# Optimization experiments

Measured on AMD Instinct MI355X. Metric: run time of the kernel, lower is better.

The kernel has to match this reference:

```python
import jax, jax.numpy as jnp
import numpy as np

KERNEL = 11  # matches AttnBlock(kernel_size=11)
EPS = 1e-4


def _patches(x, k):
    """Extract k x k patches (stride 1, VALID), matching nn.Unfold ordering.

    x: [B, C, H, W] -> ([B, L, C*k*k], (Hp, Wp)) with L = Hp*Wp.
    """
    p = jax.lax.conv_general_dilated_patches(x, (k, k), (1, 1), 'VALID')  # [B, C*k*k, Hp, Wp]
    B, D, Hp, Wp = p.shape
    return p.reshape(B, D, Hp * Wp).transpose(0, 2, 1), (Hp, Wp)


def setup_inputs() -> dict:
    key = jax.random.key(0)
    k1, k2 = jax.random.split(key)
    im1 = jax.random.normal(k1, (4, 64, 40, 40), dtype=jnp.float32)
    im2 = jax.random.normal(k2, (4, 64, 40, 40), dtype=jnp.float32)
    return {"im1": im1, "im2": im2}


def reference(im1, im2):
    k = KERNEL
    # Dynamic per-sample filters from im1 patches, L2-normalized per patch.
    p1, _ = _patches(im1, k)                                  # [B, L, D], D = C*k*k
    norm = jnp.sqrt(jnp.sum(p1 * p1, axis=-1, keepdims=True))  # [B, L, 1]
    p1n = p1 / jnp.maximum(norm, EPS)
    # conv2d(im2, filters) with stride 1 / no padding == dot of im2 patches with filters.
    p2, (Hp, Wp) = _patches(im2, k)                           # [B, P, D], P = Hp*Wp
    scores = jnp.einsum('bld,bpd->bpl', p1n, p2)              # [B, P, L]
    out = jnp.max(scores, axis=-1)                            # max over filter (channel) dim
    B = im1.shape[0]
    return out.reshape(B, 1, Hp, Wp)
```

## Files before the change

kernel.cpp:

```cpp
#include <hip/hip_runtime.h>

#define C_    64
#define H_    40
#define W_    40
#define KS    11
#define HP    30
#define NB    4
#define NL    900
#define ND    59
#define EPSF  1e-4f
#define PCH   6
#define SCW   65
#define SCB   33
#define NINF  -3.4e38f
#define MPAD  1664
#define GSTEP 66600

typedef _Float16 f16x8 __attribute__((ext_vector_type(8)));
typedef float    f32x4 __attribute__((ext_vector_type(4)));

__global__ __launch_bounds__(128)
void k_pack(const float* __restrict__ im2, const float* __restrict__ im1,
            _Float16* __restrict__ packed, float* __restrict__ ssqbuf,
            unsigned int* __restrict__ keys) {
    const int blk = blockIdx.x, b = blockIdx.y, img = blockIdx.z;
    const int pos = blk * 128 + threadIdx.x;
    const float* src = (img ? im1 : im2) + b * C_ * 1600;
    _Float16* dst = packed + ((size_t)img * NB + b) * (8 * MPAD * 8);
    float ss = 0.f;
    #pragma unroll
    for (int oct = 0; oct < 8; ++oct) {
        f16x8 h = {};
        if (pos < 1600) {
            #pragma unroll
            for (int j = 0; j < 8; ++j) {
                float v = src[(oct * 8 + j) * 1600 + pos];
                h[j] = (_Float16)v;
                ss += v * v;
            }
        }
        *(f16x8*)&dst[(oct * MPAD + pos) * 8] = h;
    }
    if (img == 1 && pos < 1600) ssqbuf[b * 1600 + pos] = ss;
    if (img == 0 && pos < NL) keys[b * NL + pos] = 0u;
}

__global__ __launch_bounds__(256, 3)
void k_gram(const _Float16* __restrict__ packed, _Float16* __restrict__ G,
            const float* __restrict__ ssqbuf, float* __restrict__ invnorm) {
    const int i = blockIdx.x, j = blockIdx.y, b = blockIdx.z;
    const int tid = threadIdx.x;
    __shared__ __align__(16) _Float16 smem[128 * 136];

    int dd = i - j; if (dd < 0) dd = -dd;
    if (dd > 10) {
        if (i < j) {
            const int part = (j == 11) ? 0 : ((i == 0) ? 1 : 2);
            const int ly0 = part * 10;
            float* ssq = (float*)smem;
            float* colsum = ssq + 800;
            for (int t = tid; t < 800; t += 256)
                ssq[t] = ssqbuf[b * 1600 + ly0 * W_ + t];
            __syncthreads();
            for (int t = tid; t < 10 * W_; t += 256) {
                int yy = t / W_, x = t - yy * W_;
                float s = 0.f;
                #pragma unroll
                for (int r = 0; r < KS; ++r) s += ssq[(yy + r) * W_ + x];
                colsum[t] = s;
            }
            __syncthreads();
            for (int t = tid; t < 10 * HP; t += 256) {
                int ly = t / HP, lx = t - ly * HP;
                float s = 0.f;
                #pragma unroll
                for (int sx = 0; sx < KS; ++sx) s += colsum[ly * W_ + lx + sx];
                invnorm[b * NL + (ly0 + ly) * HP + lx] = 1.f / fmaxf(sqrtf(s), EPSF);
            }
        }
        return;
    }
    const int w = tid >> 6, L = tid & 63, lq = L >> 4, lr = L & 15;

    _Float16 (*As)[128][8] = (_Float16 (*)[128][8])smem;
    _Float16 (*Bs)[128][8] = (_Float16 (*)[128][8])(smem + 8192);

    const _Float16* pa = packed + (size_t)b * (8 * MPAD * 8);
    const _Float16* pb = packed + (size_t)(NB + b) * (8 * MPAD * 8);
    for (int t = tid; t < 1024; t += 256) {
        int oct = t >> 7, m = t & 127;
        *(f16x8*)&As[oct][m][0] = *(const f16x8*)&pa[(oct * MPAD + i * 128 + m) * 8];
        *(f16x8*)&Bs[oct][m][0] = *(const f16x8*)&pb[(oct * MPAD + j * 128 + m) * 8];
    }
    __syncthreads();

    const int mb = (w & 1) * 64, nb = (w >> 1) * 64;
    f16x8 a0[4], a1[4], b0[4], b1[4];
    #pragma unroll
    for (int q = 0; q < 4; ++q) {
        a0[q] = *(const f16x8*)&As[lq][mb + q * 16 + lr][0];
        a1[q] = *(const f16x8*)&As[4 + lq][mb + q * 16 + lr][0];
        b0[q] = *(const f16x8*)&Bs[lq][nb + q * 16 + lr][0];
        b1[q] = *(const f16x8*)&Bs[4 + lq][nb + q * 16 + lr][0];
    }
    f32x4 acc[4][4];
    #pragma unroll
    for (int mi = 0; mi < 4; ++mi)
        #pragma unroll
        for (int ni = 0; ni < 4; ++ni) {
            f32x4 c = {0.f, 0.f, 0.f, 0.f};
            c = __builtin_amdgcn_mfma_f32_16x16x32_f16(a0[mi], b0[ni], c, 0, 0, 0);
            c = __builtin_amdgcn_mfma_f32_16x16x32_f16(a1[mi], b1[ni], c, 0, 0, 0);
            acc[mi][ni] = c;
        }
    __syncthreads();
    #pragma unroll
    for (int mi = 0; mi < 4; ++mi)
        #pragma unroll
        for (int ni = 0; ni < 4; ++ni)
            #pragma unroll
            for (int rg = 0; rg < 4; ++rg)
                smem[(mb + mi * 16 + lq * 4 + rg) * 136 + nb + ni * 16 + lr] =
                    (_Float16)acc[mi][ni][rg];
    __syncthreads();
    _Float16* Gb = G + (size_t)b * (MPAD * MPAD);
    for (int t = tid; t < 2048; t += 256) {
        int row = t >> 4, seg = t & 15;
        *(f16x8*)&Gb[(size_t)(i * 128 + row) * MPAD + j * 128 + seg * 8] =
            *(const f16x8*)&smem[row * 136 + seg * 8];
    }
}

__global__ __launch_bounds__(256, 4)
void k_box(const _Float16* __restrict__ G, const float* __restrict__ invnorm,
           unsigned int* __restrict__ keys) {
    const int chunk = blockIdx.x;
    const int dy = (int)blockIdx.y - (HP - 1);
    const int b = blockIdx.z;
    const int ady = dy < 0 ? -dy : dy;
    const int rows = HP - ady;
    if (chunk * PCH >= rows) return;
    const int pyLo = dy < 0 ? -dy : 0;
    const int py0 = pyLo + chunk * PCH;
    const int P = min(PCH, rows - chunk * PCH);
    const int tid = threadIdx.x;

    __shared__ float csum[1600];
    __shared__ float scratch[HP * SCB];
    __shared__ float sInvAll[PCH][HP];

    if (tid < P * HP) {
        int i = tid / HP, lx = tid - i * HP;
        sInvAll[i][lx] = invnorm[b * NL + (py0 + i + dy) * HP + lx];
    }

    const _Float16* Gb = G + (size_t)b * (MPAD * MPAD);
    float s[8];
    f16x8 qa, qs;
    const _Float16* base = nullptr;
    if (tid < 200) {
        int e = tid * 8, x2 = e / 40, x1 = e - x2 * 40;
        base = Gb + (size_t)py0 * GSTEP + x2 * MPAD + dy * 40 + x1;
        #pragma unroll
        for (int j = 0; j < 8; ++j) s[j] = 0.f;
        for (int r = 0; r < KS; ++r) {
            f16x8 q = *(const f16x8*)(base + r * GSTEP);
            #pragma unroll
            for (int j = 0; j < 8; ++j) s[j] += (float)q[j];
        }
    }

    for (int i = 0; i < P; ++i) {
        const int py = py0 + i;
        if (tid < 200) {
            if (i > 0) {
                #pragma unroll
                for (int j = 0; j < 8; ++j) s[j] += (float)qa[j] - (float)qs[j];
            }
            float4* c4 = (float4*)(csum + tid * 8);
            c4[0] = make_float4(s[0], s[1], s[2], s[3]);
            c4[1] = make_float4(s[4], s[5], s[6], s[7]);
            if (i + 1 < P) {
                qa = *(const f16x8*)(base + (i + 11) * GSTEP);
                qs = *(const f16x8*)(base + i * GSTEP);
            }
        }
        __syncthreads();
        for (int t = tid; t < 5 * ND; t += 256) {
            int pg = t / ND, dxI = t - ND * pg;
            int dx = dxI - (HP - 1), pxb = 6 * pg;
            int u0 = max(0, -dx - pxb), u1 = min(5, (HP - 1) - dx - pxb);
            if (u0 <= u1) {
                const float* cp = csum + dx;
                float run = 0.f;
                #pragma unroll
                for (int sr = 0; sr < KS; ++sr) run += cp[(pxb + u0 + sr) * (W_ + 1)];
                int u = u0;
                for (;;) {
                    int px = pxb + u;
                    scratch[px * SCB + px + dx] = run;
                    if (++u > u1) break;
                    run += cp[(pxb + u + 10) * (W_ + 1)] - cp[(pxb + u - 1) * (W_ + 1)];
                }
            }
        }
        __syncthreads();
        if (tid < 240) {
            int px = tid >> 3, l = tid & 7;
            const float* srow = scratch + px * SCB;
            const float* inv = sInvAll[i];
            float m = NINF;
            #pragma unroll
            for (int k = 0; k < 4; ++k) {
                int lx = l + 8 * k;
                if (lx < HP) m = fmaxf(m, srow[lx] * inv[lx]);
            }
            m = fmaxf(m, __shfl_xor(m, 1));
            m = fmaxf(m, __shfl_xor(m, 2));
            m = fmaxf(m, __shfl_xor(m, 4));
            if (l == 0) {
                unsigned int ub = __float_as_uint(m);
                unsigned int k = (ub & 0x80000000u) ? ~ub : (ub | 0x80000000u);
                atomicMax(&keys[b * NL + py * HP + px], k);
            }
        }
    }
}

__global__ __launch_bounds__(256)
void k_decode(const unsigned int* __restrict__ keys, float* __restrict__ out) {
    int i = blockIdx.x * 256 + threadIdx.x;
    if (i < NB * NL) {
        unsigned int k = keys[i];
        unsigned int u = (k & 0x80000000u) ? (k ^ 0x80000000u) : ~k;
        out[i] = __uint_as_float(u);
    }
}

__global__ __launch_bounds__(256)
void k_norm_fb(const float* __restrict__ im1, float* __restrict__ invnorm) {
    const int ly = blockIdx.x, b = blockIdx.y;
    const int tid = threadIdx.x;
    __shared__ float colsq[KS * W_];
    __shared__ float colsum[W_];
    const float* base = im1 + b * C_ * H_ * W_;
    for (int i = tid; i < KS * W_; i += 256) {
        int r = i / W_, x = i - r * W_;
        const float* p = base + (ly + r) * W_ + x;
        float s = 0.f;
        #pragma unroll 8
        for (int c = 0; c < C_; ++c) { float v = p[c * H_ * W_]; s += v * v; }
        colsq[i] = s;
    }
    __syncthreads();
    if (tid < W_) {
        float s = 0.f;
        #pragma unroll
        for (int r = 0; r < KS; ++r) s += colsq[r * W_ + tid];
        colsum[tid] = s;
    }
    __syncthreads();
    if (tid < HP) {
        float s = 0.f;
        #pragma unroll
        for (int sx = 0; sx < KS; ++sx) s += colsum[tid + sx];
        invnorm[b * NL + ly * HP + tid] = 1.f / fmaxf(sqrtf(s), EPSF);
    }
}

#define MAXPL 16
__global__ __launch_bounds__(256, 2)
void k_main_fb(const float* __restrict__ im1, const float* __restrict__ im2,
               const float* __restrict__ invnorm, unsigned int* __restrict__ keys) {
    const int chunk = blockIdx.x;
    const int dy = (int)blockIdx.y - (HP - 1);
    const int b = blockIdx.z;
    const int ady = dy < 0 ? -dy : dy;
    const int rows = HP - ady;
    if (chunk * PCH >= rows) return;
    const int pyLo = dy < 0 ? -dy : 0;
    const int py0 = pyLo + chunk * PCH;
    const int P = min(PCH, rows - chunk * PCH);
    const int nPl = P + KS - 1;
    const int tid = threadIdx.x;
    const int w = tid >> 6, L = tid & 63, lq = L >> 4, lr = L & 15;

    __shared__ __align__(16) _Float16 planes[MAXPL][H_ * W_];
    __shared__ __align__(16) float csum[H_ * W_];
    __shared__ __align__(16) _Float16 Astg[8][48][8];
    __shared__ __align__(16) _Float16 Bstg[8][48][8];
    __shared__ float scratch[HP * SCW];
    __shared__ float partials[120];
    __shared__ float sInv[HP];

    const float* im1b = im1 + b * C_ * H_ * W_;
    const float* im2b = im2 + b * C_ * H_ * W_;
    if (tid < 128) {
        int arr = tid >> 6, r = tid & 63;
        int oct = r >> 3, x = 40 + (r & 7);
        f16x8 z = {};
        *(f16x8*)((arr ? Bstg : Astg)[oct][x]) = z;
    }
    for (int p = 0; p < nPl; ++p) {
        const int y = py0 + p;
        for (int t = tid; t < 640; t += 256) {
            int arr = t >= 320;
            int r = arr ? t - 320 : t;
            int oct = r / 40, x = r - oct * 40;
            const float* pc = (arr ? (im1b + (y + dy) * W_) : (im2b + y * W_))
                              + oct * 8 * H_ * W_ + x;
            f16x8 h;
            #pragma unroll
            for (int j = 0; j < 8; ++j) h[j] = (_Float16)pc[j * H_ * W_];
            *(f16x8*)((arr ? Bstg : Astg)[oct][x]) = h;
        }
        __syncthreads();
        for (int t = w; t < 9; t += 4) {
            int mt = t / 3, nt = t - 3 * mt;
            f16x8 a0 = *(const f16x8*)(Astg[lq][mt * 16 + lr]);
            f16x8 b0 = *(const f16x8*)(Bstg[lq][nt * 16 + lr]);
            f16x8 a1 = *(const f16x8*)(Astg[4 + lq][mt * 16 + lr]);
            f16x8 b1 = *(const f16x8*)(Bstg[4 + lq][nt * 16 + lr]);
            f32x4 acc = {0.f, 0.f, 0.f, 0.f};
            acc = __builtin_amdgcn_mfma_f32_16x16x32_f16(a0, b0, acc, 0, 0, 0);
            acc = __builtin_amdgcn_mfma_f32_16x16x32_f16(a1, b1, acc, 0, 0, 0);
            int x1 = nt * 16 + lr;
            if (x1 < W_) {
                int x2b = mt * 16 + lq * 4;
                #pragma unroll
                for (int rg = 0; rg < 4; ++rg) {
                    int x2 = x2b + rg;
                    if (x2 < W_) planes[p][x2 * W_ + x1] = (_Float16)acc[rg];
                }
            }
        }
        __syncthreads();
    }
    for (int i = 0; i < P; ++i) {
        const int py = py0 + i, ly = py + dy;
        if (tid < 200) {
            float4* c4 = (float4*)(csum + tid * 8);
            if (i == 0) {
                float s[8] = {0.f,0.f,0.f,0.f,0.f,0.f,0.f,0.f};
                #pragma unroll
                for (int r = 0; r < KS; ++r) {
                    f16x8 q = *(const f16x8*)(planes[r] + tid * 8);
                    #pragma unroll
                    for (int j = 0; j < 8; ++j) s[j] += (float)q[j];
                }
                c4[0] = make_float4(s[0], s[1], s[2], s[3]);
                c4[1] = make_float4(s[4], s[5], s[6], s[7]);
            } else {
                f16x8 qa = *(const f16x8*)(planes[i + 10] + tid * 8);
                f16x8 qs = *(const f16x8*)(planes[i - 1] + tid * 8);
                float4 v0 = c4[0], v1 = c4[1];
                v0.x += (float)qa[0] - (float)qs[0]; v0.y += (float)qa[1] - (float)qs[1];
                v0.z += (float)qa[2] - (float)qs[2]; v0.w += (float)qa[3] - (float)qs[3];
                v1.x += (float)qa[4] - (float)qs[4]; v1.y += (float)qa[5] - (float)qs[5];
                v1.z += (float)qa[6] - (float)qs[6]; v1.w += (float)qa[7] - (float)qs[7];
                c4[0] = v0; c4[1] = v1;
            }
        } else if (tid >= 224 && tid < 224 + HP) {
            sInv[tid - 224] = invnorm[b * NL + ly * HP + (tid - 224)];
        }
        __syncthreads();
        for (int t = tid; t < 5 * ND; t += 256) {
            int pg = t / ND, dxI = t - ND * pg;
            int dx = dxI - (HP - 1), pxb = 6 * pg;
            #pragma unroll
            for (int u = 0; u < 6; ++u) scratch[(pxb + u) * SCW + dxI] = NINF;
            int u0 = max(0, -dx - pxb), u1 = min(5, (HP - 1) - dx - pxb);
            if (u0 <= u1) {
                const float* cp = csum + dx;
                float run = 0.f;
                #pragma unroll
                for (int sr = 0; sr < KS; ++sr) run += cp[(pxb + u0 + sr) * (W_ + 1)];
                int u = u0;
                for (;;) {
                    scratch[(pxb + u) * SCW + dxI] = run * sInv[pxb + u + dx];
                    if (++u > u1) break;
                    run += cp[(pxb + u + 10) * (W_ + 1)] - cp[(pxb + u - 1) * (W_ + 1)];
                }
            }
        }
        __syncthreads();
        if (tid < 120) {
            int px = tid >> 2, q = tid & 3;
            float m = NINF;
            int d0 = q * 15, d1 = min(d0 + 15, ND);
            for (int d = d0; d < d1; ++d) m = fmaxf(m, scratch[px * SCW + d]);
            partials[tid] = m;
        }
        __syncthreads();
        if (tid < HP) {
            float m = fmaxf(fmaxf(partials[tid * 4], partials[tid * 4 + 1]),
                            fmaxf(partials[tid * 4 + 2], partials[tid * 4 + 3]));
            unsigned int ub = __float_as_uint(m);
            unsigned int k = (ub & 0x80000000u) ? ~ub : (ub | 0x80000000u);
            atomicMax(&keys[b * NL + py * HP + tid], k);
        }
        __syncthreads();
    }
}

extern "C" void kernel_launch(void* const* d_in, const int* in_sizes, int n_in,
                              void* d_out, int out_size, void* d_ws, size_t ws_size,
                              hipStream_t stream) {
    const float* im1 = (const float*)d_in[0];
    const float* im2 = (const float*)d_in[1];
    unsigned int* keys = (unsigned int*)d_ws;
    float* invnorm = (float*)((char*)d_ws + 14400);
    float* ssqbuf  = (float*)((char*)d_ws + 28800);
    const size_t packedOff = 65536;
    const size_t packedBytes = (size_t)2 * NB * 8 * MPAD * 8 * 2;
    const size_t gOff = packedOff + packedBytes;
    const size_t gBytes = (size_t)NB * MPAD * MPAD * 2;
    const size_t needed = gOff + gBytes;

    if (ws_size >= needed) {
        _Float16* packed = (_Float16*)((char*)d_ws + packedOff);
        _Float16* G = (_Float16*)((char*)d_ws + gOff);
        k_pack<<<dim3(13, NB, 2), 128, 0, stream>>>(im2, im1, packed, ssqbuf, keys);
        k_gram<<<dim3(13, 13, NB), 256, 0, stream>>>(packed, G, ssqbuf, invnorm);
        k_box<<<dim3(5, ND, NB), 256, 0, stream>>>(G, invnorm, keys);
    } else {
        hipMemsetAsync(d_ws, 0, NB * NL * sizeof(unsigned int), stream);
        k_norm_fb<<<dim3(HP, NB), 256, 0, stream>>>(im1, invnorm);
        k_main_fb<<<dim3(5, ND, NB), 256, 0, stream>>>(im1, im2, invnorm, keys);
    }
    k_decode<<<(NB * NL + 255) / 256, 256, 0, stream>>>(keys, (float*)d_out);
}
```

Before: 98.26 us.

## Fuse pack into gram, fold decode into box via last-block counter

Removes the separate fp16 pack kernel: the gram kernel now converts fp32 inputs to fp16 directly into shared memory, and its off-diagonal blocks compute the sum of squares and zero the keys. The decode kernel is folded into the box kernel through a global atomic counter, so the last block to finish writes the output. The box kernel's dx-column work is also repartitioned into 4 groups of 8/7 pixels instead of 5 groups of 6. This cuts kernel launches and the packed intermediate buffer, but each gram tile now reads strided fp32 data redundantly, and the last-block decode is serial.

```diff
diff --git a/kernel.cpp b/kernel.cpp
--- a/kernel.cpp
+++ b/kernel.cpp
@@ -15,39 +15,15 @@
 #define NINF  -3.4e38f
 #define MPAD  1664
 #define GSTEP 66600
+#define TOTALB (5 * ND * NB)
 
 typedef _Float16 f16x8 __attribute__((ext_vector_type(8)));
 typedef float    f32x4 __attribute__((ext_vector_type(4)));
 
-__global__ __launch_bounds__(128)
-void k_pack(const float* __restrict__ im2, const float* __restrict__ im1,
-            _Float16* __restrict__ packed, float* __restrict__ ssqbuf,
-            unsigned int* __restrict__ keys) {
-    const int blk = blockIdx.x, b = blockIdx.y, img = blockIdx.z;
-    const int pos = blk * 128 + threadIdx.x;
-    const float* src = (img ? im1 : im2) + b * C_ * 1600;
-    _Float16* dst = packed + ((size_t)img * NB + b) * (8 * MPAD * 8);
-    float ss = 0.f;
-    #pragma unroll
-    for (int oct = 0; oct < 8; ++oct) {
-        f16x8 h = {};
-        if (pos < 1600) {
-            #pragma unroll
-            for (int j = 0; j < 8; ++j) {
-                float v = src[(oct * 8 + j) * 1600 + pos];
-                h[j] = (_Float16)v;
-                ss += v * v;
-            }
-        }
-        *(f16x8*)&dst[(oct * MPAD + pos) * 8] = h;
-    }
-    if (img == 1 && pos < 1600) ssqbuf[b * 1600 + pos] = ss;
-    if (img == 0 && pos < NL) keys[b * NL + pos] = 0u;
-}
-
 __global__ __launch_bounds__(256, 3)
-void k_gram(const _Float16* __restrict__ packed, _Float16* __restrict__ G,
-            const float* __restrict__ ssqbuf, float* __restrict__ invnorm) {
+void k_gram2(const float* __restrict__ im2, const float* __restrict__ im1,
+             _Float16* __restrict__ G, float* __restrict__ invnorm,
+             unsigned int* __restrict__ keys, unsigned int* __restrict__ counter) {
     const int i = blockIdx.x, j = blockIdx.y, b = blockIdx.z;
     const int tid = threadIdx.x;
     __shared__ __align__(16) _Float16 smem[128 * 136];
@@ -59,8 +35,16 @@
             const int ly0 = part * 10;
             float* ssq = (float*)smem;
             float* colsum = ssq + 800;
-            for (int t = tid; t < 800; t += 256)
-                ssq[t] = ssqbuf[b * 1600 + ly0 * W_ + t];
+            const float* im1b = im1 + b * C_ * 1600;
+            if (tid < 200) {
+                f32x4 acc = {0.f, 0.f, 0.f, 0.f};
+                const float* p = im1b + ly0 * W_ + tid * 4;
+                for (int c = 0; c < C_; ++c) {
+                    f32x4 v = *(const f32x4*)(p + c * 1600);
+                    acc += v * v;
+                }
+                *(f32x4*)&ssq[tid * 4] = acc;
+            }
             __syncthreads();
             for (int t = tid; t < 10 * W_; t += 256) {
                 int yy = t / W_, x = t - yy * W_;
@@ -77,6 +61,11 @@
                 for (int sx = 0; sx < KS; ++sx) s += colsum[ly * W_ + lx + sx];
                 invnorm[b * NL + (ly0 + ly) * HP + lx] = 1.f / fmaxf(sqrtf(s), EPSF);
             }
+        } else {
+            const int part = (i == 11) ? 0 : ((j == 0) ? 1 : 2);
+            for (int t = tid; t < 300; t += 256)
+                keys[b * NL + part * 300 + t] = 0u;
+            if (part == 0 && b == 0 && tid == 0) *counter = 0u;
         }
         return;
     }
@@ -85,12 +74,28 @@
     _Float16 (*As)[128][8] = (_Float16 (*)[128][8])smem;
     _Float16 (*Bs)[128][8] = (_Float16 (*)[128][8])(smem + 8192);
 
-    const _Float16* pa = packed + (size_t)b * (8 * MPAD * 8);
-    const _Float16* pb = packed + (size_t)(NB + b) * (8 * MPAD * 8);
-    for (int t = tid; t < 1024; t += 256) {
-        int oct = t >> 7, m = t & 127;
-        *(f16x8*)&As[oct][m][0] = *(const f16x8*)&pa[(oct * MPAD + i * 128 + m) * 8];
-        *(f16x8*)&Bs[oct][m][0] = *(const f16x8*)&pb[(oct * MPAD + j * 128 + m) * 8];
+    {
+        const float* src2 = im2 + b * C_ * 1600;
+        const float* src1 = im1 + b * C_ * 1600;
+        const int half = tid >> 7, m = tid & 127;
+        const int posA = i * 128 + m, posB = j * 128 + m;
+        #pragma unroll
+        for (int q = 0; q < 4; ++q) {
+            const int oct = half * 4 + q;
+            f16x8 ha = {}, hb = {};
+            if (posA < 1600) {
+                #pragma unroll
+                for (int jj = 0; jj < 8; ++jj)
+                    ha[jj] = (_Float16)src2[(oct * 8 + jj) * 1600 + posA];
+            }
+            if (posB < 1600) {
+                #pragma unroll
+                for (int jj = 0; jj < 8; ++jj)
+                    hb[jj] = (_Float16)src1[(oct * 8 + jj) * 1600 + posB];
+            }
+            *(f16x8*)&As[oct][m][0] = ha;
+            *(f16x8*)&Bs[oct][m][0] = hb;
+        }
     }
     __syncthreads();
 
@@ -131,27 +136,23 @@
     }
 }
 
-__global__ __launch_bounds__(256, 4)
-void k_box(const _Float16* __restrict__ G, const float* __restrict__ invnorm,
-           unsigned int* __restrict__ keys) {
-    const int chunk = blockIdx.x;
-    const int dy = (int)blockIdx.y - (HP - 1);
-    const int b = blockIdx.z;
+__device__ __forceinline__ void dev_box(int chunk, int dy, int b, int tid,
+        float* __restrict__ smemf,
+        const _Float16* __restrict__ G, const float* __restrict__ invnorm,
+        unsigned int* __restrict__ keys) {
     const int ady = dy < 0 ? -dy : dy;
     const int rows = HP - ady;
-    if (chunk * PCH >= rows) return;
     const int pyLo = dy < 0 ? -dy : 0;
     const int py0 = pyLo + chunk * PCH;
     const int P = min(PCH, rows - chunk * PCH);
-    const int tid = threadIdx.x;
-
-    __shared__ float csum[1600];
-    __shared__ float scratch[HP * SCB];
-    __shared__ float sInvAll[PCH][HP];
+
+    float* csum    = smemf;
+    float* scratch = smemf + 1600;
+    float* sInv    = smemf + 1600 + HP * SCB;
 
     if (tid < P * HP) {
         int i = tid / HP, lx = tid - i * HP;
-        sInvAll[i][lx] = invnorm[b * NL + (py0 + i + dy) * HP + lx];
+        sInv[i * HP + lx] = invnorm[b * NL + (py0 + i + dy) * HP + lx];
     }
 
     const _Float16* Gb = G + (size_t)b * (MPAD * MPAD);
@@ -186,10 +187,12 @@
             }
         }
         __syncthreads();
-        for (int t = tid; t < 5 * ND; t += 256) {
-            int pg = t / ND, dxI = t - ND * pg;
-            int dx = dxI - (HP - 1), pxb = 6 * pg;
-            int u0 = max(0, -dx - pxb), u1 = min(5, (HP - 1) - dx - pxb);
+        if (tid < 4 * ND) {
+            int pg = tid / ND, dxI = tid - ND * pg;
+            int dx = dxI - (HP - 1);
+            int pxb = (pg < 2) ? (pg << 3) : (16 + (pg - 2) * 7);
+            int usz = (pg < 2) ? 8 : 7;
+            int u0 = max(0, -dx - pxb), u1 = min(usz - 1, (HP - 1) - dx - pxb);
             if (u0 <= u1) {
                 const float* cp = csum + dx;
                 float run = 0.f;
@@ -208,7 +211,7 @@
         if (tid < 240) {
             int px = tid >> 3, l = tid & 7;
             const float* srow = scratch + px * SCB;
-            const float* inv = sInvAll[i];
+            const float* inv = sInv + i * HP;
             float m = NINF;
             #pragma unroll
             for (int k = 0; k < 4; ++k) {
@@ -223,6 +226,36 @@
                 unsigned int k = (ub & 0x80000000u) ? ~ub : (ub | 0x80000000u);
                 atomicMax(&keys[b * NL + py * HP + px], k);
             }
+        }
+    }
+}
+
+__global__ __launch_bounds__(256, 4)
+void k_box2(const _Float16* __restrict__ G, const float* __restrict__ invnorm,
+            unsigned int* __restrict__ keys, float* __restrict__ out,
+            unsigned int* __restrict__ counter) {
+    __shared__ __align__(16) float smemf[1600 + HP * SCB + PCH * HP];
+    __shared__ unsigned int lastFlag;
+    const int chunk = blockIdx.x;
+    const int dy = (int)blockIdx.y - (HP - 1);
+    const int b = blockIdx.z;
+    const int ady = dy < 0 ? -dy : dy;
+    const int tid = threadIdx.x;
+
+    if (chunk * PCH < HP - ady)
+        dev_box(chunk, dy, b, tid, smemf, G, invnorm, keys);
+
+    __syncthreads();
+    if (tid == 0) {
+        __threadfence();
+        lastFlag = (atomicAdd(counter, 1u) == (unsigned int)(TOTALB - 1)) ? 1u : 0u;
+    }
+    __syncthreads();
+    if (lastFlag) {
+        for (int t = tid; t < NB * NL; t += 256) {
+            unsigned int k = atomicMax(&keys[t], 0u);
+            unsigned int u = (k & 0x80000000u) ? (k ^ 0x80000000u) : ~k;
+            out[t] = __uint_as_float(u);
         }
     }
 }
@@ -410,23 +443,19 @@
     const float* im2 = (const float*)d_in[1];
     unsigned int* keys = (unsigned int*)d_ws;
     float* invnorm = (float*)((char*)d_ws + 14400);
-    float* ssqbuf  = (float*)((char*)d_ws + 28800);
-    const size_t packedOff = 65536;
-    const size_t packedBytes = (size_t)2 * NB * 8 * MPAD * 8 * 2;
-    const size_t gOff = packedOff + packedBytes;
+    unsigned int* counter = (unsigned int*)((char*)d_ws + 28800);
+    const size_t gOff = 65536;
     const size_t gBytes = (size_t)NB * MPAD * MPAD * 2;
     const size_t needed = gOff + gBytes;
 
     if (ws_size >= needed) {
-        _Float16* packed = (_Float16*)((char*)d_ws + packedOff);
         _Float16* G = (_Float16*)((char*)d_ws + gOff);
-        k_pack<<<dim3(13, NB, 2), 128, 0, stream>>>(im2, im1, packed, ssqbuf, keys);
-        k_gram<<<dim3(13, 13, NB), 256, 0, stream>>>(packed, G, ssqbuf, invnorm);
-        k_box<<<dim3(5, ND, NB), 256, 0, stream>>>(G, invnorm, keys);
+        k_gram2<<<dim3(13, 13, NB), 256, 0, stream>>>(im2, im1, G, invnorm, keys, counter);
+        k_box2<<<dim3(5, ND, NB), 256, 0, stream>>>(G, invnorm, keys, (float*)d_out, counter);
     } else {
         hipMemsetAsync(d_ws, 0, NB * NL * sizeof(unsigned int), stream);
         k_norm_fb<<<dim3(HP, NB), 256, 0, stream>>>(im1, invnorm);
         k_main_fb<<<dim3(5, ND, NB), 256, 0, stream>>>(im1, im2, invnorm, keys);
-    }
-    k_decode<<<(NB * NL + 255) / 256, 256, 0, stream>>>(keys, (float*)d_out);
-}
+        k_decode<<<(NB * NL + 255) / 256, 256, 0, stream>>>(keys, (float*)d_out);
+    }
+}
```

Result: slower. 117.7 us (+19.8%).

## Fuse decode into box kernel via last-block counter, remap blocks per XCD

Applied to the files above, without the earlier changes.

The separate decode launch is folded into the box kernel: each block bumps a global counter, and the last block to finish decodes all keys into the output. Blocks are remapped from a flat grid so that consecutive logical work is grouped onto the same XCD, which is meant to improve L2 locality on the G matrix. The sliding row sum keeps the first five loaded rows in registers so it no longer reloads the subtracted row. The column box-sum pass is split into 4 px-groups instead of 5 so it fits in one pass of threads. The trade-off is a serial tail in which one block decodes 3600 values, plus extra atomic and fence cost in every block.

```diff
diff --git a/kernel.cpp b/kernel.cpp
--- a/kernel.cpp
+++ b/kernel.cpp
@@ -15,6 +15,7 @@
 #define NINF  -3.4e38f
 #define MPAD  1664
 #define GSTEP 66600
+#define TOTALB (5 * ND * NB)
 
 typedef _Float16 f16x8 __attribute__((ext_vector_type(8)));
 typedef float    f32x4 __attribute__((ext_vector_type(4)));
@@ -22,7 +23,7 @@
 __global__ __launch_bounds__(128)
 void k_pack(const float* __restrict__ im2, const float* __restrict__ im1,
             _Float16* __restrict__ packed, float* __restrict__ ssqbuf,
-            unsigned int* __restrict__ keys) {
+            unsigned int* __restrict__ keys, unsigned int* __restrict__ counter) {
     const int blk = blockIdx.x, b = blockIdx.y, img = blockIdx.z;
     const int pos = blk * 128 + threadIdx.x;
     const float* src = (img ? im1 : im2) + b * C_ * 1600;
@@ -43,6 +44,7 @@
     }
     if (img == 1 && pos < 1600) ssqbuf[b * 1600 + pos] = ss;
     if (img == 0 && pos < NL) keys[b * NL + pos] = 0u;
+    if (img == 0 && b == 0 && pos == 1600) *counter = 0u;
 }
 
 __global__ __launch_bounds__(256, 3)
@@ -132,97 +134,131 @@
 }
 
 __global__ __launch_bounds__(256, 4)
-void k_box(const _Float16* __restrict__ G, const float* __restrict__ invnorm,
-           unsigned int* __restrict__ keys) {
-    const int chunk = blockIdx.x;
-    const int dy = (int)blockIdx.y - (HP - 1);
-    const int b = blockIdx.z;
+void k_box3(const _Float16* __restrict__ G, const float* __restrict__ invnorm,
+            unsigned int* __restrict__ keys, float* __restrict__ out,
+            unsigned int* __restrict__ counter) {
+    __shared__ float smemf[1600 + HP * SCB + PCH * HP];
+    __shared__ unsigned int lastFlag;
+    const int tid = threadIdx.x;
+
+    const int p = blockIdx.x;
+    const int xcd = p & 7, slot = p >> 3;
+    const int q = TOTALB / 8, r = TOTALB % 8;
+    const int logical = (xcd < r) ? (xcd * (q + 1) + slot)
+                                  : (r * (q + 1) + (xcd - r) * q + slot);
+    const int b = logical / 295;
+    const int rem = logical - b * 295;
+    const int dyI = rem / 5, chunk = rem - dyI * 5;
+    const int dy = dyI - (HP - 1);
     const int ady = dy < 0 ? -dy : dy;
     const int rows = HP - ady;
-    if (chunk * PCH >= rows) return;
-    const int pyLo = dy < 0 ? -dy : 0;
-    const int py0 = pyLo + chunk * PCH;
-    const int P = min(PCH, rows - chunk * PCH);
-    const int tid = threadIdx.x;
-
-    __shared__ float csum[1600];
-    __shared__ float scratch[HP * SCB];
-    __shared__ float sInvAll[PCH][HP];
-
-    if (tid < P * HP) {
-        int i = tid / HP, lx = tid - i * HP;
-        sInvAll[i][lx] = invnorm[b * NL + (py0 + i + dy) * HP + lx];
-    }
-
-    const _Float16* Gb = G + (size_t)b * (MPAD * MPAD);
-    float s[8];
-    f16x8 qa, qs;
-    const _Float16* base = nullptr;
-    if (tid < 200) {
-        int e = tid * 8, x2 = e / 40, x1 = e - x2 * 40;
-        base = Gb + (size_t)py0 * GSTEP + x2 * MPAD + dy * 40 + x1;
+
+    if (chunk * PCH < rows) {
+        const int pyLo = dy < 0 ? -dy : 0;
+        const int py0 = pyLo + chunk * PCH;
+        const int P = min(PCH, rows - chunk * PCH);
+
+        float* csum    = smemf;
+        float* scratch = smemf + 1600;
+        float* sInv    = smemf + 1600 + HP * SCB;
+
+        if (tid < P * HP) {
+            int i = tid / HP, lx = tid - i * HP;
+            sInv[i * HP + lx] = invnorm[b * NL + (py0 + i + dy) * HP + lx];
+        }
+
+        const _Float16* Gb = G + (size_t)b * (MPAD * MPAD);
+        float s[8];
+        f16x8 ring[5], nxt;
+        const _Float16* base = nullptr;
+        if (tid < 200) {
+            int e = tid * 8, x2 = e / 40, x1 = e - x2 * 40;
+            base = Gb + (size_t)py0 * GSTEP + x2 * MPAD + dy * 40 + x1;
+            #pragma unroll
+            for (int j = 0; j < 8; ++j) s[j] = 0.f;
+            #pragma unroll
+            for (int r2 = 0; r2 < KS; ++r2) {
+                f16x8 qv = *(const f16x8*)(base + r2 * GSTEP);
+                #pragma unroll
+                for (int j = 0; j < 8; ++j) s[j] += (float)qv[j];
+                if (r2 < 5) ring[r2] = qv;
+            }
+        }
+
         #pragma unroll
-        for (int j = 0; j < 8; ++j) s[j] = 0.f;
-        for (int r = 0; r < KS; ++r) {
-            f16x8 q = *(const f16x8*)(base + r * GSTEP);
-            #pragma unroll
-            for (int j = 0; j < 8; ++j) s[j] += (float)q[j];
-        }
-    }
-
-    for (int i = 0; i < P; ++i) {
-        const int py = py0 + i;
-        if (tid < 200) {
-            if (i > 0) {
-                #pragma unroll
-                for (int j = 0; j < 8; ++j) s[j] += (float)qa[j] - (float)qs[j];
-            }
-            float4* c4 = (float4*)(csum + tid * 8);
-            c4[0] = make_float4(s[0], s[1], s[2], s[3]);
-            c4[1] = make_float4(s[4], s[5], s[6], s[7]);
-            if (i + 1 < P) {
-                qa = *(const f16x8*)(base + (i + 11) * GSTEP);
-                qs = *(const f16x8*)(base + i * GSTEP);
-            }
-        }
-        __syncthreads();
-        for (int t = tid; t < 5 * ND; t += 256) {
-            int pg = t / ND, dxI = t - ND * pg;
-            int dx = dxI - (HP - 1), pxb = 6 * pg;
-            int u0 = max(0, -dx - pxb), u1 = min(5, (HP - 1) - dx - pxb);
-            if (u0 <= u1) {
-                const float* cp = csum + dx;
-                float run = 0.f;
-                #pragma unroll
-                for (int sr = 0; sr < KS; ++sr) run += cp[(pxb + u0 + sr) * (W_ + 1)];
-                int u = u0;
-                for (;;) {
-                    int px = pxb + u;
-                    scratch[px * SCB + px + dx] = run;
-                    if (++u > u1) break;
-                    run += cp[(pxb + u + 10) * (W_ + 1)] - cp[(pxb + u - 1) * (W_ + 1)];
-                }
-            }
-        }
-        __syncthreads();
-        if (tid < 240) {
-            int px = tid >> 3, l = tid & 7;
-            const float* srow = scratch + px * SCB;
-            const float* inv = sInvAll[i];
-            float m = NINF;
-            #pragma unroll
-            for (int k = 0; k < 4; ++k) {
-                int lx = l + 8 * k;
-                if (lx < HP) m = fmaxf(m, srow[lx] * inv[lx]);
-            }
-            m = fmaxf(m, __shfl_xor(m, 1));
-            m = fmaxf(m, __shfl_xor(m, 2));
-            m = fmaxf(m, __shfl_xor(m, 4));
-            if (l == 0) {
-                unsigned int ub = __float_as_uint(m);
-                unsigned int k = (ub & 0x80000000u) ? ~ub : (ub | 0x80000000u);
-                atomicMax(&keys[b * NL + py * HP + px], k);
-            }
+        for (int i = 0; i < PCH; ++i) {
+            if (i < P) {
+                const int py = py0 + i;
+                if (tid < 200) {
+                    if (i > 0) {
+                        #pragma unroll
+                        for (int j = 0; j < 8; ++j)
+                            s[j] += (float)nxt[j] - (float)ring[i - 1][j];
+                    }
+                    float4* c4 = (float4*)(csum + tid * 8);
+                    c4[0] = make_float4(s[0], s[1], s[2], s[3]);
+                    c4[1] = make_float4(s[4], s[5], s[6], s[7]);
+                    if (i + 1 < P)
+                        nxt = *(const f16x8*)(base + (i + 11) * GSTEP);
+                }
+                __syncthreads();
+                if (tid < 4 * ND) {
+                    int pg = tid / ND, dxI = tid - ND * pg;
+                    int dx = dxI - (HP - 1);
+                    int pxb = (pg < 2) ? (pg << 3) : (16 + (pg - 2) * 7);
+                    int usz = (pg < 2) ? 8 : 7;
+                    int u0 = max(0, -dx - pxb), u1 = min(usz - 1, (HP - 1) - dx - pxb);
+                    if (u0 <= u1) {
+                        const float* cp = csum + dx;
+                        float run = 0.f;
+                        #pragma unroll
+                        for (int sr = 0; sr < KS; ++sr)
+                            run += cp[(pxb + u0 + sr) * (W_ + 1)];
+                        int u = u0;
+                        for (;;) {
+                            int px = pxb + u;
+                            scratch[px * SCB + px + dx] = run;
+                            if (++u > u1) break;
+                            run += cp[(pxb + u + 10) * (W_ + 1)]
+                                 - cp[(pxb + u - 1) * (W_ + 1)];
+                        }
+                    }
+                }
+                __syncthreads();
+                if (tid < 240) {
+                    int px = tid >> 3, l = tid & 7;
+                    const float* srow = scratch + px * SCB;
+                    const float* inv = sInv + i * HP;
+                    float m = NINF;
+                    #pragma unroll
+                    for (int k = 0; k < 4; ++k) {
+                        int lx = l + 8 * k;
+                        if (lx < HP) m = fmaxf(m, srow[lx] * inv[lx]);
+                    }
+                    m = fmaxf(m, __shfl_xor(m, 1));
+                    m = fmaxf(m, __shfl_xor(m, 2));
+                    m = fmaxf(m, __shfl_xor(m, 4));
+                    if (l == 0) {
+                        unsigned int ub = __float_as_uint(m);
+                        unsigned int k = (ub & 0x80000000u) ? ~ub : (ub | 0x80000000u);
+                        atomicMax(&keys[b * NL + py * HP + px], k);
+                    }
+                }
+            }
+        }
+    }
+
+    __syncthreads();
+    if (tid == 0) {
+        __threadfence();
+        lastFlag = (atomicAdd(counter, 1u) == (unsigned int)(TOTALB - 1)) ? 1u : 0u;
+    }
+    __syncthreads();
+    if (lastFlag) {
+        for (int t = tid; t < NB * NL; t += 256) {
+            unsigned int k = atomicMax(&keys[t], 0u);
+            unsigned int u = (k & 0x80000000u) ? (k ^ 0x80000000u) : ~k;
+            out[t] = __uint_as_float(u);
         }
     }
 }
@@ -411,6 +447,7 @@
     unsigned int* keys = (unsigned int*)d_ws;
     float* invnorm = (float*)((char*)d_ws + 14400);
     float* ssqbuf  = (float*)((char*)d_ws + 28800);
+    unsigned int* counter = (unsigned int*)((char*)d_ws + 54400);
     const size_t packedOff = 65536;
     const size_t packedBytes = (size_t)2 * NB * 8 * MPAD * 8 * 2;
     const size_t gOff = packedOff + packedBytes;
@@ -420,13 +457,13 @@
     if (ws_size >= needed) {
         _Float16* packed = (_Float16*)((char*)d_ws + packedOff);
         _Float16* G = (_Float16*)((char*)d_ws + gOff);
-        k_pack<<<dim3(13, NB, 2), 128, 0, stream>>>(im2, im1, packed, ssqbuf, keys);
+        k_pack<<<dim3(13, NB, 2), 128, 0, stream>>>(im2, im1, packed, ssqbuf, keys, counter);
         k_gram<<<dim3(13, 13, NB), 256, 0, stream>>>(packed, G, ssqbuf, invnorm);
-        k_box<<<dim3(5, ND, NB), 256, 0, stream>>>(G, invnorm, keys);
+        k_box3<<<dim3(TOTALB), 256, 0, stream>>>(G, invnorm, keys, (float*)d_out, counter);
     } else {
         hipMemsetAsync(d_ws, 0, NB * NL * sizeof(unsigned int), stream);
         k_norm_fb<<<dim3(HP, NB), 256, 0, stream>>>(im1, invnorm);
         k_main_fb<<<dim3(5, ND, NB), 256, 0, stream>>>(im1, im2, invnorm, keys);
-    }
-    k_decode<<<(NB * NL + 255) / 256, 256, 0, stream>>>(keys, (float*)d_out);
-}
+        k_decode<<<(NB * NL + 255) / 256, 256, 0, stream>>>(keys, (float*)d_out);
+    }
+}
```

Result: slower. 111.5 us (+13.5%).
